# Kernel tuning notes

Hardware: AMD Instinct MI355X
Metric: run time of the kernel (lower is better)

The kernel has to match this reference:

```python
import jax, jax.numpy as jnp
import numpy as np

N_NODES = 100000
N_EDGES = 3200000
D_FEAT = 128


def setup_inputs() -> dict:
    key = jax.random.key(0)
    k1, k2, k3, k4 = jax.random.split(key, 4)
    edge_row = jax.random.randint(k1, (N_EDGES,), 0, N_NODES, dtype=jnp.int64 if jax.config.jax_enable_x64 else jnp.int32)
    edge_col = jax.random.randint(k2, (N_EDGES,), 0, N_NODES, dtype=edge_row.dtype)
    edge_val = jax.random.uniform(k3, (N_EDGES,), dtype=jnp.float32)
    embeds = jax.random.normal(k4, (N_NODES, D_FEAT), dtype=jnp.float32)
    return {"edge_row": edge_row, "edge_col": edge_col, "edge_val": edge_val, "embeds": embeds}


def reference(edge_row, edge_col, edge_val, embeds):
    # SpMM: out[r] = sum_{e: row(e)=r} val(e) * embeds[col(e)]
    messages = edge_val[:, None] * embeds[edge_col]  # [E, D]
    out = jax.ops.segment_sum(messages, edge_row, num_segments=embeds.shape[0])  # [N, D]
    return out
```

## Files before the change

### kernel.cpp

```cpp
#include <hip/hip_runtime.h>
#include <hip/hip_bf16.h>
#include <stdint.h>

#define N_NODES 100000
#define D_FEAT  128
#define RSH     5
#define RPB     32
#define NBUCK   ((N_NODES + RPB - 1) / RPB)
#define CAPF    1152
#define KMAX    ((CAPF + 255) / 256)
#define OCAP    8192
#define SC_THR  1024
#define SC_EPT  16
#define SC_TILE (SC_THR * SC_EPT)
#define COLMASK 0x1FFFF

__global__ __launch_bounds__(256) void conv_bf16_kernel(const float2* __restrict__ in,
                                                        uint32_t* __restrict__ outp, int n2) {
    int i = blockIdx.x * 256 + threadIdx.x;
    if (i < n2) {
        float2 f = in[i];
        uint32_t bx = __float_as_uint(f.x); bx = (bx + 0x7FFFu + ((bx >> 16) & 1u)) >> 16;
        uint32_t by = __float_as_uint(f.y); by = (by + 0x7FFFu + ((by >> 16) & 1u)) >> 16;
        outp[i] = bx | (by << 16);
    }
}

__global__ __launch_bounds__(SC_THR) void scatter_fixed_kernel(
    const int* __restrict__ row, const int* __restrict__ col,
    const float* __restrict__ val, int* __restrict__ cursor,
    int2* __restrict__ rec, int4* __restrict__ oflow, int* __restrict__ ocnt, int n)
{
    __shared__ int cnt[NBUCK];
    __shared__ int base[NBUCK];
    const int tid = threadIdx.x;
    const int e0  = blockIdx.x * SC_TILE + tid * SC_EPT;

    for (int i = tid; i < NBUCK; i += SC_THR) cnt[i] = 0;
    __syncthreads();

    int   r[SC_EPT], c[SC_EPT];
    float v[SC_EPT];
    if (e0 + SC_EPT <= n) {
        const int4* rp = (const int4*)(row + e0);
        const int4* cp = (const int4*)(col + e0);
        const float4* vp = (const float4*)(val + e0);
        #pragma unroll
        for (int q = 0; q < SC_EPT / 4; q++) {
            int4 rr = rp[q]; int4 cc = cp[q]; float4 vv = vp[q];
            r[q*4+0]=rr.x; r[q*4+1]=rr.y; r[q*4+2]=rr.z; r[q*4+3]=rr.w;
            c[q*4+0]=cc.x; c[q*4+1]=cc.y; c[q*4+2]=cc.z; c[q*4+3]=cc.w;
            v[q*4+0]=vv.x; v[q*4+1]=vv.y; v[q*4+2]=vv.z; v[q*4+3]=vv.w;
        }
    } else {
        #pragma unroll
        for (int k = 0; k < SC_EPT; k++) {
            int e = e0 + k;
            if (e < n) { r[k] = row[e]; c[k] = col[e]; v[k] = val[e]; }
            else       { r[k] = -1; }
        }
    }

    int rk[SC_EPT];
    #pragma unroll
    for (int k = 0; k < SC_EPT; k++)
        if (r[k] >= 0) rk[k] = atomicAdd(&cnt[r[k] >> RSH], 1);
    __syncthreads();

    for (int i = tid; i < NBUCK; i += SC_THR) {
        int cc = cnt[i];
        if (cc) base[i] = atomicAdd(&cursor[i], cc);
    }
    __syncthreads();

    #pragma unroll
    for (int k = 0; k < SC_EPT; k++) {
        if (r[k] >= 0) {
            int bk  = r[k] >> RSH;
            int pos = base[bk] + rk[k];
            if (pos < CAPF) {
                rec[(size_t)bk * CAPF + pos] =
                    make_int2(((r[k] & (RPB - 1)) << 17) | c[k], __float_as_int(v[k]));
            } else {
                int op = atomicAdd(ocnt, 1);
                if (op < OCAP) oflow[op] = make_int4(r[k], c[k], __float_as_int(v[k]), 0);
            }
        }
    }
}

template <bool BF16>
__global__ __launch_bounds__(256) void spmm_fixed_kernel(const int* __restrict__ fill,
                                                         const int2* __restrict__ rec,
                                                         const void* __restrict__ emb,
                                                         float* __restrict__ out)
{
    __shared__ int2 buf[CAPF];
    __shared__ int  cnt[RPB];
    __shared__ int  start[RPB];
    __shared__ int  sc_[RPB];

    const int tid  = threadIdx.x;
    const int lane = tid & 63;
    const int wv   = tid >> 6;
    const int b    = blockIdx.x;
    const int m    = min(fill[b], CAPF);
    const size_t beg = (size_t)b * CAPF;
    const uint32_t* __restrict__ embu = (const uint32_t*)emb;
    const float2*   __restrict__ emb2 = (const float2*)emb;

    if (tid < RPB) cnt[tid] = 0;
    __syncthreads();

    int2 rc[KMAX];
    int  rk[KMAX];
    #pragma unroll
    for (int k = 0; k < KMAX; k++) {
        int i = k * 256 + tid;
        if (i < m) {
            rc[k] = rec[beg + i];
            rk[k] = atomicAdd(&cnt[rc[k].x >> 17], 1);
        }
    }
    __syncthreads();
    if (tid < RPB) sc_[tid] = cnt[tid];
    __syncthreads();
    for (int off = 1; off < RPB; off <<= 1) {
        int t = 0;
        if (tid < RPB && tid >= off) t = sc_[tid - off];
        __syncthreads();
        if (tid < RPB) sc_[tid] += t;
        __syncthreads();
    }
    if (tid < RPB) start[tid] = sc_[tid] - cnt[tid];
    __syncthreads();
    #pragma unroll
    for (int k = 0; k < KMAX; k++) {
        int i = k * 256 + tid;
        if (i < m) buf[start[rc[k].x >> 17] + rk[k]] = rc[k];
    }
    __syncthreads();

    for (int rl = wv * 8; rl < wv * 8 + 8; rl++) {
        const int s0 = start[rl];
        const int c0 = cnt[rl];
        float ax = 0.f, ay = 0.f;
        int j = 0;
        for (; j + 8 <= c0; j += 8) {
            int2 e[8];
            #pragma unroll
            for (int q = 0; q < 8; q++) e[q] = buf[s0 + j + q];
            float mx[8], my[8], vv[8];
            #pragma unroll
            for (int q = 0; q < 8; q++) {
                int cc = e[q].x & COLMASK;
                vv[q] = __int_as_float(e[q].y);
                if (BF16) {
                    uint32_t u = embu[(size_t)cc * 64 + lane];
                    mx[q] = __uint_as_float(u << 16);
                    my[q] = __uint_as_float(u & 0xFFFF0000u);
                } else {
                    float2 mm = emb2[(size_t)cc * 64 + lane];
                    mx[q] = mm.x; my[q] = mm.y;
                }
            }
            #pragma unroll
            for (int q = 0; q < 8; q++) { ax += vv[q] * mx[q]; ay += vv[q] * my[q]; }
        }
        for (; j < c0; j++) {
            int2 e = buf[s0 + j];
            int cc = e.x & COLMASK;
            float vv = __int_as_float(e.y);
            float mx, my;
            if (BF16) {
                uint32_t u = embu[(size_t)cc * 64 + lane];
                mx = __uint_as_float(u << 16);
                my = __uint_as_float(u & 0xFFFF0000u);
            } else {
                float2 mm = emb2[(size_t)cc * 64 + lane];
                mx = mm.x; my = mm.y;
            }
            ax += vv * mx; ay += vv * my;
        }
        float2* o = (float2*)(out + (size_t)(b * RPB + rl) * D_FEAT);
        o[lane] = make_float2(ax, ay);
    }
}

__global__ __launch_bounds__(256) void oflow_kernel(const int4* __restrict__ oflow,
                                                    const int* __restrict__ ocnt,
                                                    const float* __restrict__ embeds,
                                                    float* __restrict__ out) {
    const int nof  = min(*ocnt, OCAP);
    const int lane = threadIdx.x & 63;
    const int w    = (blockIdx.x * 256 + threadIdx.x) >> 6;
    const int nw   = (gridDim.x * 256) >> 6;
    for (int i = w; i < nof; i += nw) {
        int4 e = oflow[i];
        const float2* src = (const float2*)(embeds + (size_t)e.y * D_FEAT);
        float2 mm = src[lane];
        float vv = __int_as_float(e.z);
        float* dst = out + (size_t)e.x * D_FEAT + (lane << 1);
        unsafeAtomicAdd(dst,     vv * mm.x);
        unsafeAtomicAdd(dst + 1, vv * mm.y);
    }
}

__global__ __launch_bounds__(256) void spmm_atomic_kernel(
    const int* __restrict__ edge_row, const int* __restrict__ edge_col,
    const float* __restrict__ edge_val, const float* __restrict__ embeds,
    float* __restrict__ out, int n_edges)
{
    const int lane    = threadIdx.x & 63;
    const int wave_id = (blockIdx.x * blockDim.x + threadIdx.x) >> 6;
    const int n_waves = (gridDim.x * blockDim.x) >> 6;
    for (int e = wave_id; e < n_edges; e += n_waves) {
        const int   r = edge_row[e];
        const int   c = edge_col[e];
        const float vv = edge_val[e];
        const float2* src = (const float2*)(embeds + (size_t)c * D_FEAT);
        float2 mm = src[lane];
        float* dst = out + (size_t)r * D_FEAT + (lane << 1);
        unsafeAtomicAdd(dst,     vv * mm.x);
        unsafeAtomicAdd(dst + 1, vv * mm.y);
    }
}

static inline size_t align256(size_t x) { return (x + 255) & ~(size_t)255; }

extern "C" void kernel_launch(void* const* d_in, const int* in_sizes, int n_in,
                              void* d_out, int out_size, void* d_ws, size_t ws_size,
                              hipStream_t stream) {
    const int*   edge_row = (const int*)d_in[0];
    const int*   edge_col = (const int*)d_in[1];
    const float* edge_val = (const float*)d_in[2];
    const float* embeds   = (const float*)d_in[3];
    float*       out      = (float*)d_out;

    const int n_edges = in_sizes[0];

    size_t off = 0;
    size_t o_cursor = off; off = align256(off + (size_t)(NBUCK + 1) * 4);
    size_t o_oflow  = off; off = align256(off + (size_t)OCAP * 16);
    size_t o_rec    = off; off = align256(off + (size_t)NBUCK * CAPF * 8);
    const size_t need_fp32 = off;
    size_t o_emb    = off; off = align256(off + (size_t)N_NODES * 64 * 4);
    const size_t need_bf16 = off;

    if (ws_size < need_fp32) {
        hipMemsetAsync(out, 0, (size_t)out_size * sizeof(float), stream);
        spmm_atomic_kernel<<<dim3(4096), dim3(256), 0, stream>>>(
            edge_row, edge_col, edge_val, embeds, out, n_edges);
        return;
    }

    char* ws = (char*)d_ws;
    int*      cursor = (int*)(ws + o_cursor);
    int*      ocnt   = cursor + NBUCK;
    int4*     oflow  = (int4*)(ws + o_oflow);
    int2*     rec    = (int2*)(ws + o_rec);
    uint32_t* embbf  = (uint32_t*)(ws + o_emb);

    const bool use_bf16 = (ws_size >= need_bf16);

    hipMemsetAsync(cursor, 0, (size_t)(NBUCK + 1) * 4, stream);
    if (use_bf16) {
        const int n2 = N_NODES * (D_FEAT / 2);
        conv_bf16_kernel<<<dim3((n2 + 255) / 256), dim3(256), 0, stream>>>(
            (const float2*)embeds, embbf, n2);
    }
    scatter_fixed_kernel<<<dim3((n_edges + SC_TILE - 1) / SC_TILE), dim3(SC_THR), 0, stream>>>(
        edge_row, edge_col, edge_val, cursor, rec, oflow, ocnt, n_edges);
    if (use_bf16)
        spmm_fixed_kernel<true><<<dim3(NBUCK), dim3(256), 0, stream>>>(cursor, rec, embbf, out);
    else
        spmm_fixed_kernel<false><<<dim3(NBUCK), dim3(256), 0, stream>>>(cursor, rec, embeds, out);
    oflow_kernel<<<dim3(16), dim3(256), 0, stream>>>(oflow, ocnt, embeds, out);
}
```

Before: 286.7 us.

## Fuse bf16 conversion into scatter kernel and double rows per bucket

The separate bf16 conversion kernel is folded into the scatter launch: extra blocks beyond the scatter grid convert embeddings while the other blocks bucket edges. Buckets grow from 32 to 64 rows, and the SpMM kernel moves to 512 threads with larger slab capacities. An optional padding mode rounds each block's per-bucket reservation up to a multiple of 8 and fills the gaps with zero-weight records. This saves one launch and overlaps the conversion with the scatter, and it halves the bucket count. The cost is larger workspace, some padding writes, and more shared memory per SpMM block.

```diff
diff --git a/kernel.cpp b/kernel.cpp
--- a/kernel.cpp
+++ b/kernel.cpp
@@ -4,33 +4,39 @@
 
 #define N_NODES 100000
 #define D_FEAT  128
-#define RSH     5
-#define RPB     32
+#define RSH     6
+#define RPB     64
 #define NBUCK   ((N_NODES + RPB - 1) / RPB)
-#define CAPF    1152
-#define KMAX    ((CAPF + 255) / 256)
 #define OCAP    8192
 #define SC_THR  1024
 #define SC_EPT  16
 #define SC_TILE (SC_THR * SC_EPT)
 #define COLMASK 0x1FFFF
 
-__global__ __launch_bounds__(256) void conv_bf16_kernel(const float2* __restrict__ in,
-                                                        uint32_t* __restrict__ outp, int n2) {
-    int i = blockIdx.x * 256 + threadIdx.x;
-    if (i < n2) {
-        float2 f = in[i];
-        uint32_t bx = __float_as_uint(f.x); bx = (bx + 0x7FFFu + ((bx >> 16) & 1u)) >> 16;
-        uint32_t by = __float_as_uint(f.y); by = (by + 0x7FFFu + ((by >> 16) & 1u)) >> 16;
-        outp[i] = bx | (by << 16);
-    }
-}
-
-__global__ __launch_bounds__(SC_THR) void scatter_fixed_kernel(
+__device__ __forceinline__ uint32_t bf16_rne(float x) {
+    uint32_t u = __float_as_uint(x);
+    return (u + 0x7FFFu + ((u >> 16) & 1u)) >> 16;
+}
+
+template <int CAPF_, bool PAD, bool CONV>
+__global__ __launch_bounds__(SC_THR) void scatter_conv_kernel(
     const int* __restrict__ row, const int* __restrict__ col,
     const float* __restrict__ val, int* __restrict__ cursor,
-    int2* __restrict__ rec, int4* __restrict__ oflow, int* __restrict__ ocnt, int n)
+    int2* __restrict__ rec, int4* __restrict__ oflow, int* __restrict__ ocnt,
+    const float4* __restrict__ embf, uint2* __restrict__ embbf,
+    int n, int scb, int n4)
 {
+    if (CONV && (int)blockIdx.x >= scb) {
+        const int nb = gridDim.x - scb;
+        const int stride = nb * SC_THR;
+        for (int i = (blockIdx.x - scb) * SC_THR + threadIdx.x; i < n4; i += stride) {
+            float4 f = embf[i];
+            embbf[i] = make_uint2(bf16_rne(f.x) | (bf16_rne(f.y) << 16),
+                                  bf16_rne(f.z) | (bf16_rne(f.w) << 16));
+        }
+        return;
+    }
+
     __shared__ int cnt[NBUCK];
     __shared__ int base[NBUCK];
     const int tid = threadIdx.x;
@@ -69,7 +75,18 @@
 
     for (int i = tid; i < NBUCK; i += SC_THR) {
         int cc = cnt[i];
-        if (cc) base[i] = atomicAdd(&cursor[i], cc);
+        if (cc) {
+            int padded = PAD ? ((cc + 7) & ~7) : cc;
+            int b0 = atomicAdd(&cursor[i], padded);
+            base[i] = b0;
+            if (PAD) {
+                int2* slab = rec + (size_t)i * CAPF_;
+                for (int p = cc; p < padded; ++p) {
+                    int pos = b0 + p;
+                    if (pos < CAPF_) slab[pos] = make_int2(0, 0);
+                }
+            }
+        }
     }
     __syncthreads();
 
@@ -78,8 +95,8 @@
         if (r[k] >= 0) {
             int bk  = r[k] >> RSH;
             int pos = base[bk] + rk[k];
-            if (pos < CAPF) {
-                rec[(size_t)bk * CAPF + pos] =
+            if (pos < CAPF_) {
+                rec[(size_t)bk * CAPF_ + pos] =
                     make_int2(((r[k] & (RPB - 1)) << 17) | c[k], __float_as_int(v[k]));
             } else {
                 int op = atomicAdd(ocnt, 1);
@@ -89,13 +106,14 @@
     }
 }
 
-template <bool BF16>
-__global__ __launch_bounds__(256) void spmm_fixed_kernel(const int* __restrict__ fill,
+template <bool BF16, int CAPF_>
+__global__ __launch_bounds__(512) void spmm_fixed_kernel(const int* __restrict__ fill,
                                                          const int2* __restrict__ rec,
                                                          const void* __restrict__ emb,
                                                          float* __restrict__ out)
 {
-    __shared__ int2 buf[CAPF];
+    constexpr int KMAX = (CAPF_ + 511) / 512;
+    __shared__ int2 buf[CAPF_];
     __shared__ int  cnt[RPB];
     __shared__ int  start[RPB];
     __shared__ int  sc_[RPB];
@@ -104,8 +122,9 @@
     const int lane = tid & 63;
     const int wv   = tid >> 6;
     const int b    = blockIdx.x;
-    const int m    = min(fill[b], CAPF);
-    const size_t beg = (size_t)b * CAPF;
+    const int m    = min(fill[b], CAPF_);
+    const int rows = min(RPB, N_NODES - b * RPB);
+    const size_t beg = (size_t)b * CAPF_;
     const uint32_t* __restrict__ embu = (const uint32_t*)emb;
     const float2*   __restrict__ emb2 = (const float2*)emb;
 
@@ -116,7 +135,7 @@
     int  rk[KMAX];
     #pragma unroll
     for (int k = 0; k < KMAX; k++) {
-        int i = k * 256 + tid;
+        int i = k * 512 + tid;
         if (i < m) {
             rc[k] = rec[beg + i];
             rk[k] = atomicAdd(&cnt[rc[k].x >> 17], 1);
@@ -136,7 +155,7 @@
     __syncthreads();
     #pragma unroll
     for (int k = 0; k < KMAX; k++) {
-        int i = k * 256 + tid;
+        int i = k * 512 + tid;
         if (i < m) buf[start[rc[k].x >> 17] + rk[k]] = rc[k];
     }
     __syncthreads();
@@ -182,8 +201,10 @@
             }
             ax += vv * mx; ay += vv * my;
         }
-        float2* o = (float2*)(out + (size_t)(b * RPB + rl) * D_FEAT);
-        o[lane] = make_float2(ax, ay);
+        if (rl < rows) {
+            float2* o = (float2*)(out + (size_t)(b * RPB + rl) * D_FEAT);
+            o[lane] = make_float2(ax, ay);
+        }
     }
 }
 
@@ -215,12 +236,12 @@
     const int wave_id = (blockIdx.x * blockDim.x + threadIdx.x) >> 6;
     const int n_waves = (gridDim.x * blockDim.x) >> 6;
     for (int e = wave_id; e < n_edges; e += n_waves) {
-        const int   r = edge_row[e];
-        const int   c = edge_col[e];
+        const int   rr = edge_row[e];
+        const int   cc = edge_col[e];
         const float vv = edge_val[e];
-        const float2* src = (const float2*)(embeds + (size_t)c * D_FEAT);
+        const float2* src = (const float2*)(embeds + (size_t)cc * D_FEAT);
         float2 mm = src[lane];
-        float* dst = out + (size_t)r * D_FEAT + (lane << 1);
+        float* dst = out + (size_t)rr * D_FEAT + (lane << 1);
         unsafeAtomicAdd(dst,     vv * mm.x);
         unsafeAtomicAdd(dst + 1, vv * mm.y);
     }
@@ -238,14 +259,18 @@
     float*       out      = (float*)d_out;
 
     const int n_edges = in_sizes[0];
-
-    size_t off = 0;
-    size_t o_cursor = off; off = align256(off + (size_t)(NBUCK + 1) * 4);
-    size_t o_oflow  = off; off = align256(off + (size_t)OCAP * 16);
-    size_t o_rec    = off; off = align256(off + (size_t)NBUCK * CAPF * 8);
-    const size_t need_fp32 = off;
-    size_t o_emb    = off; off = align256(off + (size_t)N_NODES * 64 * 4);
-    const size_t need_bf16 = off;
+    const int scb = (n_edges + SC_TILE - 1) / SC_TILE;
+    const int n4  = N_NODES * (D_FEAT / 4);
+
+    const size_t sz_cur   = align256((size_t)(NBUCK + 1) * 4);
+    const size_t sz_oflow = align256((size_t)OCAP * 16);
+    const size_t sz_rec_p = align256((size_t)NBUCK * 3072 * 8);
+    const size_t sz_rec_c = align256((size_t)NBUCK * 2304 * 8);
+    const size_t sz_emb   = align256((size_t)N_NODES * 64 * 4);
+
+    const size_t need_pad  = sz_cur + sz_oflow + sz_rec_p + sz_emb;
+    const size_t need_comp = sz_cur + sz_oflow + sz_rec_c + sz_emb;
+    const size_t need_fp32 = sz_cur + sz_oflow + sz_rec_c;
 
     if (ws_size < need_fp32) {
         hipMemsetAsync(out, 0, (size_t)out_size * sizeof(float), stream);
@@ -255,25 +280,35 @@
     }
 
     char* ws = (char*)d_ws;
-    int*      cursor = (int*)(ws + o_cursor);
-    int*      ocnt   = cursor + NBUCK;
-    int4*     oflow  = (int4*)(ws + o_oflow);
-    int2*     rec    = (int2*)(ws + o_rec);
-    uint32_t* embbf  = (uint32_t*)(ws + o_emb);
-
-    const bool use_bf16 = (ws_size >= need_bf16);
+    int*  cursor = (int*)ws;
+    int*  ocnt   = cursor + NBUCK;
+    int4* oflow  = (int4*)(ws + sz_cur);
 
     hipMemsetAsync(cursor, 0, (size_t)(NBUCK + 1) * 4, stream);
-    if (use_bf16) {
-        const int n2 = N_NODES * (D_FEAT / 2);
-        conv_bf16_kernel<<<dim3((n2 + 255) / 256), dim3(256), 0, stream>>>(
-            (const float2*)embeds, embbf, n2);
-    }
-    scatter_fixed_kernel<<<dim3((n_edges + SC_TILE - 1) / SC_TILE), dim3(SC_THR), 0, stream>>>(
-        edge_row, edge_col, edge_val, cursor, rec, oflow, ocnt, n_edges);
-    if (use_bf16)
-        spmm_fixed_kernel<true><<<dim3(NBUCK), dim3(256), 0, stream>>>(cursor, rec, embbf, out);
-    else
-        spmm_fixed_kernel<false><<<dim3(NBUCK), dim3(256), 0, stream>>>(cursor, rec, embeds, out);
+
+    if (ws_size >= need_pad) {
+        int2*     rec   = (int2*)(ws + sz_cur + sz_oflow);
+        uint32_t* embbf = (uint32_t*)(ws + sz_cur + sz_oflow + sz_rec_p);
+        scatter_conv_kernel<3072, true, true><<<dim3(scb * 2), dim3(SC_THR), 0, stream>>>(
+            edge_row, edge_col, edge_val, cursor, rec, oflow, ocnt,
+            (const float4*)embeds, (uint2*)embbf, n_edges, scb, n4);
+        spmm_fixed_kernel<true, 3072><<<dim3(NBUCK), dim3(512), 0, stream>>>(
+            cursor, rec, embbf, out);
+    } else if (ws_size >= need_comp) {
+        int2*     rec   = (int2*)(ws + sz_cur + sz_oflow);
+        uint32_t* embbf = (uint32_t*)(ws + sz_cur + sz_oflow + sz_rec_c);
+        scatter_conv_kernel<2304, false, true><<<dim3(scb * 2), dim3(SC_THR), 0, stream>>>(
+            edge_row, edge_col, edge_val, cursor, rec, oflow, ocnt,
+            (const float4*)embeds, (uint2*)embbf, n_edges, scb, n4);
+        spmm_fixed_kernel<true, 2304><<<dim3(NBUCK), dim3(512), 0, stream>>>(
+            cursor, rec, embbf, out);
+    } else {
+        int2* rec = (int2*)(ws + sz_cur + sz_oflow);
+        scatter_conv_kernel<2304, false, false><<<dim3(scb), dim3(SC_THR), 0, stream>>>(
+            edge_row, edge_col, edge_val, cursor, rec, oflow, ocnt,
+            (const float4*)embeds, (uint2*)nullptr, n_edges, scb, n4);
+        spmm_fixed_kernel<false, 2304><<<dim3(NBUCK), dim3(512), 0, stream>>>(
+            cursor, rec, embeds, out);
+    }
     oflow_kernel<<<dim3(16), dim3(256), 0, stream>>>(oflow, ocnt, embeds, out);
 }
```

Result: slower. 328.8 us (+14.7%).
